# Optimization experiments

Measured on AMD Instinct MI355X. Metric: run time of the kernel, lower is better.

Reference implementation:

```python
import jax, jax.numpy as jnp
import numpy as np

N, OBS, ENC, ACT, K = 16384, 512, 512, 64, 8
ALPHA = 1.0


def setup_inputs() -> dict:
    key = jax.random.key(0)
    ks = jax.random.split(key, 8)
    s = 0.05  # keep activations/logits well-scaled
    return {
        "X1": jax.random.normal(ks[0], (N, OBS), jnp.float32),
        "X0": jax.random.normal(ks[1], (N, OBS), jnp.float32),
        "U": jax.random.normal(ks[2], (N, ACT), jnp.float32),
        "W_enc": jax.random.normal(ks[3], (ENC, OBS), jnp.float32) * s,
        "A_all": jax.random.normal(ks[4], (K, ENC, ENC), jnp.float32) * s,
        "B_rest": jax.random.normal(ks[5], (K - 1, ACT, ENC), jnp.float32) * s,
        "C_w": jax.random.normal(ks[6], (K, ENC), jnp.float32) * s,
        "C_b": jax.random.normal(ks[7], (K,), jnp.float32) * s,
    }


def reference(X1, X0, U, W_enc, A_all, B_rest, C_w, C_b):
    enc_dim = W_enc.shape[0]
    act_dim = U.shape[1]
    k = A_all.shape[0]
    # encoder: bias-free linear
    X1e = X1 @ W_enc.T  # [N, enc]
    X0e = X0 @ W_enc.T  # [N, enc]
    # gating: argmax of linear classifier C
    inds = jnp.argmax(X0e @ C_w.T + C_b, axis=1)  # [N]
    # expert 0 uses fixed B0 = eye(enc)[:act, :]; experts 1..k-1 learned
    B0 = jnp.eye(enc_dim, dtype=X0.dtype)[:act_dim]  # [act, enc]
    B_all = jnp.concatenate([B0[None], B_rest], axis=0)  # [k, act, enc]
    # per-expert predictions for every row (nn.Linear: x @ W.T -> einsum over input dim h)
    preds = jnp.einsum('nh,keh->kne', X0e, A_all) + jnp.einsum('na,kae->kne', U, B_all)
    # squared error per (expert, row), then select each row's routed expert
    sq = jnp.sum((X1e[None, :, :] - preds) ** 2, axis=-1)  # [k, N]
    onehot = jax.nn.one_hot(inds, k, dtype=sq.dtype)  # [N, k]
    loss = ALPHA * jnp.sum(sq * onehot.T)
    return loss / (enc_dim * X1.shape[0])
```

## Files before the change

### kernel.cpp

```cpp
#include <hip/hip_runtime.h>

#define NROWS 16384
#define OBSD 512
#define ENCD 512
#define ACTD 64
#define KEXP 8

typedef __attribute__((ext_vector_type(8))) short bf16x8;
typedef __attribute__((ext_vector_type(4))) float f32x4;
typedef __attribute__((address_space(3))) unsigned char lds_byte;
typedef __attribute__((address_space(1))) unsigned char glb_byte;

__device__ __forceinline__ unsigned short f2bf(float f) {
  unsigned int u = __float_as_uint(f);
  u = (u + 0x7FFFu + ((u >> 16) & 1u)) >> 16;
  return (unsigned short)u;
}
__device__ __forceinline__ float bf2f(unsigned short h) {
  return __uint_as_float(((unsigned int)h) << 16);
}
__device__ __forceinline__ unsigned int cvtpk(float lo, float hi) {
  unsigned int r;
  asm("v_cvt_pk_bf16_f32 %0, %1, %2" : "=v"(r) : "v"(lo), "v"(hi));
  return r;
}
__device__ __forceinline__ void gload_lds16(const unsigned short* g, unsigned short* l) {
  __builtin_amdgcn_global_load_lds((const glb_byte*)g, (lds_byte*)l, 16, 0, 0);
}

__global__ __launch_bounds__(256) void gt_k(
    const float* __restrict__ W, const float* __restrict__ Cw,
    float* __restrict__ GT, float* __restrict__ loss,
    int* __restrict__ counts, int* __restrict__ cursor) {
  const int b = blockIdx.x, tid = threadIdx.x;
  if (b == 0) {
    if (tid == 0) *loss = 0.f;
    if (tid < KEXP) { counts[tid] = 0; cursor[tid] = 0; }
  }
  __shared__ float red[4][64];
  int e = b >> 3, o0 = (b & 7) * 64;
  int o = tid & 63, hg = tid >> 6;
  float s = 0.f;
#pragma unroll 8
  for (int h = hg * 128; h < hg * 128 + 128; h++)
    s += Cw[e * ENCD + h] * W[(size_t)h * OBSD + o0 + o];
  red[hg][o] = s;
  __syncthreads();
  if (tid < 64)
    GT[(o0 + tid) * KEXP + e] = red[0][tid] + red[1][tid] + red[2][tid] + red[3][tid];
}

__global__ __launch_bounds__(256) void fused_prep_k(
    const float* __restrict__ X0, const float* __restrict__ X1,
    const float* __restrict__ U, const float* __restrict__ W,
    const float* __restrict__ Aall, const float* __restrict__ Brest,
    const float* __restrict__ GT, const float* __restrict__ Cb,
    unsigned short* __restrict__ X0bf, unsigned short* __restrict__ X1bf,
    unsigned short* __restrict__ Ubf, unsigned short* __restrict__ Wbf,
    unsigned short* __restrict__ Abf, unsigned short* __restrict__ BfT,
    int* __restrict__ inds, int* __restrict__ counts) {
  const int b = blockIdx.x, tid = threadIdx.x;
  if (b < 512) {
    __shared__ int lhist[KEXP];
    if (tid < KEXP) lhist[tid] = 0;
    __syncthreads();
    const int lane = tid & 63, w = tid >> 6;
    float g[8][8];
    const float* gp = GT + lane * 8 * KEXP;
#pragma unroll
    for (int j = 0; j < 8; j++) {
      float4 lo = *(const float4*)(gp + j * KEXP);
      float4 hi = *(const float4*)(gp + j * KEXP + 4);
      g[j][0] = lo.x; g[j][1] = lo.y; g[j][2] = lo.z; g[j][3] = lo.w;
      g[j][4] = hi.x; g[j][5] = hi.y; g[j][6] = hi.z; g[j][7] = hi.w;
    }
    float cb[KEXP];
#pragma unroll
    for (int e = 0; e < KEXP; e++) cb[e] = Cb[e];
#pragma unroll 2
    for (int r = 0; r < 8; r++) {
      const int n = b * 32 + w * 8 + r;
      const float4* xr = (const float4*)(X0 + (size_t)n * OBSD + lane * 8);
      float4 x = xr[0], y = xr[1];
      float xv[8] = {x.x, x.y, x.z, x.w, y.x, y.y, y.z, y.w};
      float acc[KEXP] = {};
#pragma unroll
      for (int j = 0; j < 8; j++)
#pragma unroll
        for (int e = 0; e < KEXP; e++) acc[e] += xv[j] * g[j][e];
      uint4 rr = {cvtpk(x.x, x.y), cvtpk(x.z, x.w), cvtpk(y.x, y.y), cvtpk(y.z, y.w)};
      *(uint4*)&X0bf[(size_t)n * OBSD + lane * 8] = rr;
#pragma unroll
      for (int e = 0; e < KEXP; e++) {
#pragma unroll
        for (int off = 32; off > 0; off >>= 1) acc[e] += __shfl_xor(acc[e], off, 64);
      }
      if (lane == 0) {
        int best = 0;
        float bv = acc[0] + cb[0];
#pragma unroll
        for (int e = 1; e < KEXP; e++) {
          float v = acc[e] + cb[e];
          if (v > bv) { bv = v; best = e; }
        }
        inds[n] = best;
        atomicAdd(&lhist[best], 1);
      }
    }
    __syncthreads();
    if (tid < KEXP) atomicAdd(&counts[tid], lhist[tid]);
    return;
  }
  if (b < 4608) {
    size_t i = ((size_t)(b - 512) * 256 + tid) * 8;
    const float4* s4 = (const float4*)(X1 + i);
    float4 a = s4[0], c = s4[1];
    uint4 r = {cvtpk(a.x, a.y), cvtpk(a.z, a.w), cvtpk(c.x, c.y), cvtpk(c.z, c.w)};
    *(uint4*)&X1bf[i] = r;
    return;
  }
  if (b < 4664) {
    __shared__ float tile[64][65];
    int t = b - 4608;
    int k = (t >> 3);
    int e0 = (t & 7) * 64;
    const float* src = Brest + (size_t)k * ACTD * ENCD + e0;
#pragma unroll
    for (int j = 0; j < 16; j++) {
      int idx = j * 256 + tid;
      int a = idx >> 6, e = idx & 63;
      tile[a][e] = src[(size_t)a * ENCD + e];
    }
    __syncthreads();
    unsigned short* dst = BfT + ((size_t)(k + 1) * ENCD + e0) * ACTD;
#pragma unroll
    for (int j = 0; j < 16; j++) {
      int idx = j * 256 + tid;
      int e = idx >> 6, a = idx & 63;
      dst[(size_t)e * ACTD + a] = f2bf(tile[a][e]);
    }
    return;
  }
  if (b == 4664) {
    for (int j = 0; j < 16; j++) {
      int i8 = j * 256 + tid;
      int e = i8 >> 3, a0 = (i8 & 7) * 8;
      unsigned int w0 = 0, w1 = 0, w2 = 0, w3 = 0;
      if (e >= a0 && e < a0 + 8) {
        unsigned int bits = 0x3F80u << ((e & 1) * 16);
        if ((e - a0) >> 1 == 0) w0 = bits;
        else if ((e - a0) >> 1 == 1) w1 = bits;
        else if ((e - a0) >> 1 == 2) w2 = bits;
        else w3 = bits;
      }
      uint4 v = {w0, w1, w2, w3};
      *(uint4*)&BfT[(size_t)i8 * 8] = v;
    }
    return;
  }
  int cb2 = b - 4665;
  const float* src;
  unsigned short* dst;
  size_t i;
  if (cb2 < 1024)      { src = U;    dst = Ubf; i = (size_t)cb2 * 256 + tid; }
  else if (cb2 < 1280) { src = W;    dst = Wbf; i = (size_t)(cb2 - 1024) * 256 + tid; }
  else                 { src = Aall; dst = Abf; i = (size_t)(cb2 - 1280) * 256 + tid; }
  float4 v = ((const float4*)src)[i];
  uint2 r = {cvtpk(v.x, v.y), cvtpk(v.z, v.w)};
  *(uint2*)&dst[i * 4] = r;
}

__global__ void prefix_k(const int* __restrict__ counts, int* __restrict__ cursor,
                         int* __restrict__ starts) {
  if (threadIdx.x == 0 && blockIdx.x == 0) {
    int s = 0;
    for (int k = 0; k < KEXP; k++) { starts[k] = s; cursor[k] = s; s += counts[k]; }
    starts[KEXP] = s;
  }
}

__global__ __launch_bounds__(256, 2) void enc_scatter_k(
    const unsigned short* __restrict__ X1bf, const unsigned short* __restrict__ X0bf,
    const unsigned short* __restrict__ Wbf, unsigned short* __restrict__ X1e,
    unsigned short* __restrict__ X0e, const int* __restrict__ inds,
    int* __restrict__ cursor, int* __restrict__ rowlist) {
  if (blockIdx.x >= 1024) {
    __shared__ int lhist[KEXP], lbase[KEXP];
    const int tid = threadIdx.x;
    if (tid < KEXP) lhist[tid] = 0;
    __syncthreads();
    const int n = (blockIdx.x - 1024) * 256 + tid;
    const int r = inds[n];
    const int lpos = atomicAdd(&lhist[r], 1);
    __syncthreads();
    if (tid < KEXP) lbase[tid] = atomicAdd(&cursor[tid], lhist[tid]);
    __syncthreads();
    rowlist[lbase[r] + lpos] = n;
    return;
  }
  __shared__ unsigned short As[128 * 64];
  __shared__ unsigned short Bs[128 * 64];
  const int tid = threadIdx.x;
  const int bid = blockIdx.x;
  const int lid = (bid & 7) * 128 + (bid >> 3);
  const int lz = lid >> 9;
  const int rem = lid & 511;
  const int col0 = (rem & 3) * 128;
  const int row0 = (rem >> 2) * 128;
  const unsigned short* X = lz ? X0bf : X1bf;
  unsigned short* E = lz ? X0e : X1e;

  const int lane = tid & 63, w = tid >> 6;
  const int wr = w >> 1, wc = w & 1;
  const int srow8 = tid >> 3;
  const int lslot = ((tid & 7) ^ (srow8 & 7)) * 8;
  const int ldsoff = tid * 8;
  const int r15 = lane & 15;
  const int qk = lane >> 4;
  const int rsw = r15 & 7;
  const int arow = wr * 64 + r15;
  const int brow = wc * 64 + r15;

  f32x4 acc[4][4] = {};
  for (int k0 = 0; k0 < OBSD; k0 += 64) {
#pragma unroll
    for (int j = 0; j < 4; j++) {
      int row = j * 32 + srow8;
      gload_lds16(X + (size_t)(row0 + row) * OBSD + k0 + lslot, &As[j * 2048 + ldsoff]);
      gload_lds16(Wbf + (size_t)(col0 + row) * OBSD + k0 + lslot, &Bs[j * 2048 + ldsoff]);
    }
    __syncthreads();
#pragma unroll
    for (int kk = 0; kk < 2; kk++) {
      const int ps = ((kk * 4 + qk) ^ rsw) * 8;
      bf16x8 af[4], bfr[4];
#pragma unroll
      for (int m = 0; m < 4; m++) af[m] = *(const bf16x8*)&As[(arow + m * 16) * 64 + ps];
#pragma unroll
      for (int n = 0; n < 4; n++) bfr[n] = *(const bf16x8*)&Bs[(brow + n * 16) * 64 + ps];
#pragma unroll
      for (int m = 0; m < 4; m++)
#pragma unroll
        for (int n = 0; n < 4; n++)
          acc[m][n] = __builtin_amdgcn_mfma_f32_16x16x32_bf16(bfr[n], af[m], acc[m][n], 0, 0, 0);
    }
    __syncthreads();
  }
#pragma unroll
  for (int m = 0; m < 4; m++) {
    int rowg = row0 + wr * 64 + m * 16 + r15;
#pragma unroll
    for (int n = 0; n < 4; n++) {
      int colg = col0 + wc * 64 + n * 16 + qk * 4;
      uint2 v = {cvtpk(acc[m][n][0], acc[m][n][1]), cvtpk(acc[m][n][2], acc[m][n][3])};
      *(uint2*)&E[(size_t)rowg * ENCD + colg] = v;
    }
  }
}

__global__ __launch_bounds__(256, 2) void grouped_mfma_k(
    const unsigned short* __restrict__ X0ebf, const unsigned short* __restrict__ X1ebf,
    const unsigned short* __restrict__ Ubf, const unsigned short* __restrict__ Abf,
    const unsigned short* __restrict__ BfTbf, const int* __restrict__ rowlist,
    const int* __restrict__ starts, float* __restrict__ loss) {
  const int tid = threadIdx.x;
  const int bid = blockIdx.x;
  const int lid = (bid & 7) * 512 + (bid >> 3);
  const int k = lid >> 9;
  const int rem = lid & 511;
  const int col0 = (rem & 3) * 128;
  const int tile = rem >> 2;

  const int start = starts[k];
  const int cnt = starts[k + 1] - start;
  if (tile * 128 >= cnt) return;

  __shared__ unsigned short As[128 * 32];
  __shared__ unsigned short Bs[128 * 32];
  __shared__ int ridx[128];
  __shared__ float red[4];

  if (tid < 128) {
    int p = tile * 128 + tid;
    ridx[tid] = rowlist[start + (p < cnt ? p : 0)];
  }
  __syncthreads();

  const int lane = tid & 63, w = tid >> 6;
  const int wr = w >> 1, wc = w & 1;
  const int gslot = ((tid & 3) ^ ((tid >> 3) & 3)) * 8;
  const int srow = tid >> 2;
  const int ldsoff = tid * 8;
  const int rslot = ((lane >> 4) ^ (((lane & 15) >> 1) & 3)) * 8;
  const int arow = wr * 64 + (lane & 15);
  const int brow = wc * 64 + (lane & 15);
  const int rn0 = ridx[srow];
  const int rn1 = ridx[64 + srow];

  f32x4 acc[4][4] = {};
  const unsigned short* Ak = Abf + (size_t)k * ENCD * ENCD;
  for (int k0 = 0; k0 < ENCD; k0 += 32) {
    gload_lds16(X0ebf + (size_t)rn0 * ENCD + k0 + gslot, &As[ldsoff]);
    gload_lds16(X0ebf + (size_t)rn1 * ENCD + k0 + gslot, &As[2048 + ldsoff]);
    gload_lds16(Ak + (size_t)(col0 + srow) * ENCD + k0 + gslot, &Bs[ldsoff]);
    gload_lds16(Ak + (size_t)(col0 + 64 + srow) * ENCD + k0 + gslot, &Bs[2048 + ldsoff]);
    __syncthreads();
    bf16x8 af[4], bfr[4];
#pragma unroll
    for (int m = 0; m < 4; m++) af[m] = *(const bf16x8*)&As[(arow + m * 16) * 32 + rslot];
#pragma unroll
    for (int n = 0; n < 4; n++) bfr[n] = *(const bf16x8*)&Bs[(brow + n * 16) * 32 + rslot];
#pragma unroll
    for (int m = 0; m < 4; m++)
#pragma unroll
      for (int n = 0; n < 4; n++)
        acc[m][n] = __builtin_amdgcn_mfma_f32_16x16x32_bf16(bfr[n], af[m], acc[m][n], 0, 0, 0);
    __syncthreads();
  }
  const unsigned short* BfTk = BfTbf + (size_t)k * ENCD * ACTD;
  for (int a0 = 0; a0 < ACTD; a0 += 32) {
    gload_lds16(Ubf + (size_t)rn0 * ACTD + a0 + gslot, &As[ldsoff]);
    gload_lds16(Ubf + (size_t)rn1 * ACTD + a0 + gslot, &As[2048 + ldsoff]);
    gload_lds16(BfTk + (size_t)(col0 + srow) * ACTD + a0 + gslot, &Bs[ldsoff]);
    gload_lds16(BfTk + (size_t)(col0 + 64 + srow) * ACTD + a0 + gslot, &Bs[2048 + ldsoff]);
    __syncthreads();
    bf16x8 af[4], bfr[4];
#pragma unroll
    for (int m = 0; m < 4; m++) af[m] = *(const bf16x8*)&As[(arow + m * 16) * 32 + rslot];
#pragma unroll
    for (int n = 0; n < 4; n++) bfr[n] = *(const bf16x8*)&Bs[(brow + n * 16) * 32 + rslot];
#pragma unroll
    for (int m = 0; m < 4; m++)
#pragma unroll
      for (int n = 0; n < 4; n++)
        acc[m][n] = __builtin_amdgcn_mfma_f32_16x16x32_bf16(bfr[n], af[m], acc[m][n], 0, 0, 0);
    __syncthreads();
  }
  float sq = 0.f;
#pragma unroll
  for (int m = 0; m < 4; m++) {
    int lr = wr * 64 + m * 16 + (lane & 15);
    bool valid = (tile * 128 + lr) < cnt;
    const unsigned short* xrow = X1ebf + (size_t)ridx[lr] * ENCD;
#pragma unroll
    for (int n = 0; n < 4; n++) {
      int cg = col0 + wc * 64 + n * 16 + (lane >> 4) * 4;
      if (valid) {
        ushort4 x4 = *(const ushort4*)&xrow[cg];
        float d0 = bf2f(x4.x) - acc[m][n][0];
        float d1 = bf2f(x4.y) - acc[m][n][1];
        float d2 = bf2f(x4.z) - acc[m][n][2];
        float d3 = bf2f(x4.w) - acc[m][n][3];
        sq += d0 * d0 + d1 * d1 + d2 * d2 + d3 * d3;
      }
    }
  }
#pragma unroll
  for (int off = 32; off > 0; off >>= 1) sq += __shfl_xor(sq, off, 64);
  if (lane == 0) red[w] = sq;
  __syncthreads();
  if (tid == 0) atomicAdd(loss, red[0] + red[1] + red[2] + red[3]);
}

__global__ void finalize_k(const float* __restrict__ loss, float* __restrict__ out) {
  if (threadIdx.x == 0 && blockIdx.x == 0)
    out[0] = loss[0] * (1.0f / ((float)ENCD * (float)NROWS));
}

extern "C" void kernel_launch(void* const* d_in, const int* in_sizes, int n_in,
                              void* d_out, int out_size, void* d_ws, size_t ws_size,
                              hipStream_t stream) {
  const float* X1 = (const float*)d_in[0];
  const float* X0 = (const float*)d_in[1];
  const float* U = (const float*)d_in[2];
  const float* W = (const float*)d_in[3];
  const float* Aall = (const float*)d_in[4];
  const float* Brest = (const float*)d_in[5];
  const float* Cw = (const float*)d_in[6];
  const float* Cb = (const float*)d_in[7];
  float* out = (float*)d_out;

  char* p = (char*)d_ws;
  auto alloc = [&](size_t bytes) { char* r = p; p += (bytes + 255) & ~(size_t)255; return r; };
  unsigned short* X1bf = (unsigned short*)alloc((size_t)NROWS * OBSD * 2);
  unsigned short* X0bf = (unsigned short*)alloc((size_t)NROWS * OBSD * 2);
  unsigned short* Ubf = (unsigned short*)alloc((size_t)NROWS * ACTD * 2);
  unsigned short* Wbf = (unsigned short*)alloc((size_t)ENCD * OBSD * 2);
  unsigned short* Abf = (unsigned short*)alloc((size_t)KEXP * ENCD * ENCD * 2);
  unsigned short* BfT = (unsigned short*)alloc((size_t)KEXP * ENCD * ACTD * 2);
  unsigned short* X1ebf = (unsigned short*)alloc((size_t)NROWS * ENCD * 2);
  unsigned short* X0ebf = (unsigned short*)alloc((size_t)NROWS * ENCD * 2);
  float* GT = (float*)alloc(KEXP * OBSD * 4);
  float* loss = (float*)alloc(256);
  int* inds = (int*)alloc(NROWS * 4);
  int* rowlist = (int*)alloc(NROWS * 4);
  int* counts = (int*)alloc(64);
  int* cursor = (int*)alloc(64);
  int* starts = (int*)alloc(64);

  gt_k<<<64, 256, 0, stream>>>(W, Cw, GT, loss, counts, cursor);
  fused_prep_k<<<7993, 256, 0, stream>>>(X0, X1, U, W, Aall, Brest, GT, Cb,
                                         X0bf, X1bf, Ubf, Wbf, Abf, BfT,
                                         inds, counts);
  prefix_k<<<1, 1, 0, stream>>>(counts, cursor, starts);
  enc_scatter_k<<<1088, 256, 0, stream>>>(X1bf, X0bf, Wbf, X1ebf, X0ebf,
                                          inds, cursor, rowlist);
  grouped_mfma_k<<<4096, 256, 0, stream>>>(X0ebf, X1ebf, Ubf, Abf, BfT,
                                           rowlist, starts, loss);
  finalize_k<<<1, 64, 0, stream>>>(loss, out);
}
```

Measured before the change: 87.80 us.

## Fuse X1 encoding into grouped expert GEMM via negated expert weights

X1 is no longer encoded in a separate GEMM pass that writes X1e. The grouped kernel now accumulates X1@W^T, then adds X0e@(-A_k)^T and U@(-B_k)^T into the same accumulator, so the residual comes straight out of the MFMA and the loss is just its squared sum. This removes half the encoder GEMM and the X1e write and read-back, at the cost of a longer K loop per tile (OBS+ENC+ACT) and re-reading W per tile. The K-step also grows from 32 to 64 with wider swizzled LDS tiles.

Measured after the change: 83.73 us. -4.6%, faster.

```diff
diff --git a/kernel.cpp b/kernel.cpp
--- a/kernel.cpp
+++ b/kernel.cpp
@@ -15,9 +15,6 @@
   unsigned int u = __float_as_uint(f);
   u = (u + 0x7FFFu + ((u >> 16) & 1u)) >> 16;
   return (unsigned short)u;
-}
-__device__ __forceinline__ float bf2f(unsigned short h) {
-  return __uint_as_float(((unsigned int)h) << 16);
 }
 __device__ __forceinline__ unsigned int cvtpk(float lo, float hi) {
   unsigned int r;
@@ -57,7 +54,7 @@
     const float* __restrict__ GT, const float* __restrict__ Cb,
     unsigned short* __restrict__ X0bf, unsigned short* __restrict__ X1bf,
     unsigned short* __restrict__ Ubf, unsigned short* __restrict__ Wbf,
-    unsigned short* __restrict__ Abf, unsigned short* __restrict__ BfT,
+    unsigned short* __restrict__ AbfN, unsigned short* __restrict__ BfTN,
     int* __restrict__ inds, int* __restrict__ counts) {
   const int b = blockIdx.x, tid = threadIdx.x;
   if (b < 512) {
@@ -132,12 +129,12 @@
       tile[a][e] = src[(size_t)a * ENCD + e];
     }
     __syncthreads();
-    unsigned short* dst = BfT + ((size_t)(k + 1) * ENCD + e0) * ACTD;
+    unsigned short* dst = BfTN + ((size_t)(k + 1) * ENCD + e0) * ACTD;
 #pragma unroll
     for (int j = 0; j < 16; j++) {
       int idx = j * 256 + tid;
       int e = idx >> 6, a = idx & 63;
-      dst[(size_t)e * ACTD + a] = f2bf(tile[a][e]);
+      dst[(size_t)e * ACTD + a] = f2bf(-tile[a][e]);
     }
     return;
   }
@@ -147,27 +144,34 @@
       int e = i8 >> 3, a0 = (i8 & 7) * 8;
       unsigned int w0 = 0, w1 = 0, w2 = 0, w3 = 0;
       if (e >= a0 && e < a0 + 8) {
-        unsigned int bits = 0x3F80u << ((e & 1) * 16);
+        unsigned int bits = 0xBF80u << ((e & 1) * 16);
         if ((e - a0) >> 1 == 0) w0 = bits;
         else if ((e - a0) >> 1 == 1) w1 = bits;
         else if ((e - a0) >> 1 == 2) w2 = bits;
         else w3 = bits;
       }
       uint4 v = {w0, w1, w2, w3};
-      *(uint4*)&BfT[(size_t)i8 * 8] = v;
+      *(uint4*)&BfTN[(size_t)i8 * 8] = v;
     }
     return;
   }
   int cb2 = b - 4665;
-  const float* src;
-  unsigned short* dst;
-  size_t i;
-  if (cb2 < 1024)      { src = U;    dst = Ubf; i = (size_t)cb2 * 256 + tid; }
-  else if (cb2 < 1280) { src = W;    dst = Wbf; i = (size_t)(cb2 - 1024) * 256 + tid; }
-  else                 { src = Aall; dst = Abf; i = (size_t)(cb2 - 1280) * 256 + tid; }
-  float4 v = ((const float4*)src)[i];
-  uint2 r = {cvtpk(v.x, v.y), cvtpk(v.z, v.w)};
-  *(uint2*)&dst[i * 4] = r;
+  if (cb2 < 1024) {
+    size_t i = (size_t)cb2 * 256 + tid;
+    float4 v = ((const float4*)U)[i];
+    uint2 r = {cvtpk(v.x, v.y), cvtpk(v.z, v.w)};
+    *(uint2*)&Ubf[i * 4] = r;
+  } else if (cb2 < 1280) {
+    size_t i = (size_t)(cb2 - 1024) * 256 + tid;
+    float4 v = ((const float4*)W)[i];
+    uint2 r = {cvtpk(v.x, v.y), cvtpk(v.z, v.w)};
+    *(uint2*)&Wbf[i * 4] = r;
+  } else {
+    size_t i = (size_t)(cb2 - 1280) * 256 + tid;
+    float4 v = ((const float4*)Aall)[i];
+    uint2 r = {cvtpk(-v.x, -v.y), cvtpk(-v.z, -v.w)};
+    *(uint2*)&AbfN[i * 4] = r;
+  }
 }
 
 __global__ void prefix_k(const int* __restrict__ counts, int* __restrict__ cursor,
@@ -180,16 +184,15 @@
 }
 
 __global__ __launch_bounds__(256, 2) void enc_scatter_k(
-    const unsigned short* __restrict__ X1bf, const unsigned short* __restrict__ X0bf,
-    const unsigned short* __restrict__ Wbf, unsigned short* __restrict__ X1e,
+    const unsigned short* __restrict__ X0bf, const unsigned short* __restrict__ Wbf,
     unsigned short* __restrict__ X0e, const int* __restrict__ inds,
     int* __restrict__ cursor, int* __restrict__ rowlist) {
-  if (blockIdx.x >= 1024) {
+  if (blockIdx.x >= 512) {
     __shared__ int lhist[KEXP], lbase[KEXP];
     const int tid = threadIdx.x;
     if (tid < KEXP) lhist[tid] = 0;
     __syncthreads();
-    const int n = (blockIdx.x - 1024) * 256 + tid;
+    const int n = (blockIdx.x - 512) * 256 + tid;
     const int r = inds[n];
     const int lpos = atomicAdd(&lhist[r], 1);
     __syncthreads();
@@ -202,13 +205,9 @@
   __shared__ unsigned short Bs[128 * 64];
   const int tid = threadIdx.x;
   const int bid = blockIdx.x;
-  const int lid = (bid & 7) * 128 + (bid >> 3);
-  const int lz = lid >> 9;
-  const int rem = lid & 511;
-  const int col0 = (rem & 3) * 128;
-  const int row0 = (rem >> 2) * 128;
-  const unsigned short* X = lz ? X0bf : X1bf;
-  unsigned short* E = lz ? X0e : X1e;
+  const int lid = (bid & 7) * 64 + (bid >> 3);
+  const int col0 = (lid & 3) * 128;
+  const int row0 = (lid >> 2) * 128;
 
   const int lane = tid & 63, w = tid >> 6;
   const int wr = w >> 1, wc = w & 1;
@@ -226,7 +225,7 @@
 #pragma unroll
     for (int j = 0; j < 4; j++) {
       int row = j * 32 + srow8;
-      gload_lds16(X + (size_t)(row0 + row) * OBSD + k0 + lslot, &As[j * 2048 + ldsoff]);
+      gload_lds16(X0bf + (size_t)(row0 + row) * OBSD + k0 + lslot, &As[j * 2048 + ldsoff]);
       gload_lds16(Wbf + (size_t)(col0 + row) * OBSD + k0 + lslot, &Bs[j * 2048 + ldsoff]);
     }
     __syncthreads();
@@ -253,16 +252,17 @@
     for (int n = 0; n < 4; n++) {
       int colg = col0 + wc * 64 + n * 16 + qk * 4;
       uint2 v = {cvtpk(acc[m][n][0], acc[m][n][1]), cvtpk(acc[m][n][2], acc[m][n][3])};
-      *(uint2*)&E[(size_t)rowg * ENCD + colg] = v;
+      *(uint2*)&X0e[(size_t)rowg * ENCD + colg] = v;
     }
   }
 }
 
 __global__ __launch_bounds__(256, 2) void grouped_mfma_k(
-    const unsigned short* __restrict__ X0ebf, const unsigned short* __restrict__ X1ebf,
-    const unsigned short* __restrict__ Ubf, const unsigned short* __restrict__ Abf,
-    const unsigned short* __restrict__ BfTbf, const int* __restrict__ rowlist,
-    const int* __restrict__ starts, float* __restrict__ loss) {
+    const unsigned short* __restrict__ X1bf, const unsigned short* __restrict__ X0ebf,
+    const unsigned short* __restrict__ Wbf, const unsigned short* __restrict__ Ubf,
+    const unsigned short* __restrict__ AbfN, const unsigned short* __restrict__ BfTN,
+    const int* __restrict__ rowlist, const int* __restrict__ starts,
+    float* __restrict__ loss) {
   const int tid = threadIdx.x;
   const int bid = blockIdx.x;
   const int lid = (bid & 7) * 512 + (bid >> 3);
@@ -275,8 +275,8 @@
   const int cnt = starts[k + 1] - start;
   if (tile * 128 >= cnt) return;
 
-  __shared__ unsigned short As[128 * 32];
-  __shared__ unsigned short Bs[128 * 32];
+  __shared__ unsigned short As[128 * 64];
+  __shared__ unsigned short Bs[128 * 64];
   __shared__ int ridx[128];
   __shared__ float red[4];
 
@@ -288,71 +288,78 @@
 
   const int lane = tid & 63, w = tid >> 6;
   const int wr = w >> 1, wc = w & 1;
-  const int gslot = ((tid & 3) ^ ((tid >> 3) & 3)) * 8;
-  const int srow = tid >> 2;
+  const int srow8 = tid >> 3;
+  const int lslot = ((tid & 7) ^ (srow8 & 7)) * 8;
   const int ldsoff = tid * 8;
-  const int rslot = ((lane >> 4) ^ (((lane & 15) >> 1) & 3)) * 8;
-  const int arow = wr * 64 + (lane & 15);
-  const int brow = wc * 64 + (lane & 15);
-  const int rn0 = ridx[srow];
-  const int rn1 = ridx[64 + srow];
+  const int r15 = lane & 15;
+  const int qk = lane >> 4;
+  const int rsw = r15 & 7;
+  const int arow = wr * 64 + r15;
+  const int brow = wc * 64 + r15;
+  int rnj[4];
+#pragma unroll
+  for (int j = 0; j < 4; j++) rnj[j] = ridx[j * 32 + srow8];
+
+  const unsigned short* AkN = AbfN + (size_t)k * ENCD * ENCD;
+  const unsigned short* BfTkN = BfTN + (size_t)k * ENCD * ACTD;
 
   f32x4 acc[4][4] = {};
-  const unsigned short* Ak = Abf + (size_t)k * ENCD * ENCD;
-  for (int k0 = 0; k0 < ENCD; k0 += 32) {
-    gload_lds16(X0ebf + (size_t)rn0 * ENCD + k0 + gslot, &As[ldsoff]);
-    gload_lds16(X0ebf + (size_t)rn1 * ENCD + k0 + gslot, &As[2048 + ldsoff]);
-    gload_lds16(Ak + (size_t)(col0 + srow) * ENCD + k0 + gslot, &Bs[ldsoff]);
-    gload_lds16(Ak + (size_t)(col0 + 64 + srow) * ENCD + k0 + gslot, &Bs[2048 + ldsoff]);
-    __syncthreads();
-    bf16x8 af[4], bfr[4];
-#pragma unroll
-    for (int m = 0; m < 4; m++) af[m] = *(const bf16x8*)&As[(arow + m * 16) * 32 + rslot];
-#pragma unroll
-    for (int n = 0; n < 4; n++) bfr[n] = *(const bf16x8*)&Bs[(brow + n * 16) * 32 + rslot];
-#pragma unroll
-    for (int m = 0; m < 4; m++)
+#define GROUPED_COMPUTE()                                                            \
+  do {                                                                               \
+    __syncthreads();                                                                 \
+    _Pragma("unroll") for (int kk = 0; kk < 2; kk++) {                               \
+      const int ps = ((kk * 4 + qk) ^ rsw) * 8;                                      \
+      bf16x8 af[4], bfr[4];                                                          \
+      _Pragma("unroll") for (int m = 0; m < 4; m++)                                  \
+          af[m] = *(const bf16x8*)&As[(arow + m * 16) * 64 + ps];                    \
+      _Pragma("unroll") for (int n = 0; n < 4; n++)                                  \
+          bfr[n] = *(const bf16x8*)&Bs[(brow + n * 16) * 64 + ps];                   \
+      _Pragma("unroll") for (int m = 0; m < 4; m++)                                  \
+          _Pragma("unroll") for (int n = 0; n < 4; n++)                              \
+              acc[m][n] = __builtin_amdgcn_mfma_f32_16x16x32_bf16(bfr[n], af[m],     \
+                                                                  acc[m][n], 0, 0, 0); \
+    }                                                                                \
+    __syncthreads();                                                                 \
+  } while (0)
+
+  for (int k0 = 0; k0 < ENCD; k0 += 64) {
+#pragma unroll
+    for (int j = 0; j < 4; j++) {
+      int row = j * 32 + srow8;
+      gload_lds16(X1bf + (size_t)rnj[j] * OBSD + k0 + lslot, &As[j * 2048 + ldsoff]);
+      gload_lds16(Wbf + (size_t)(col0 + row) * OBSD + k0 + lslot, &Bs[j * 2048 + ldsoff]);
+    }
+    GROUPED_COMPUTE();
+  }
+  for (int k0 = 0; k0 < ENCD; k0 += 64) {
+#pragma unroll
+    for (int j = 0; j < 4; j++) {
+      int row = j * 32 + srow8;
+      gload_lds16(X0ebf + (size_t)rnj[j] * ENCD + k0 + lslot, &As[j * 2048 + ldsoff]);
+      gload_lds16(AkN + (size_t)(col0 + row) * ENCD + k0 + lslot, &Bs[j * 2048 + ldsoff]);
+    }
+    GROUPED_COMPUTE();
+  }
+  {
+#pragma unroll
+    for (int j = 0; j < 4; j++) {
+      int row = j * 32 + srow8;
+      gload_lds16(Ubf + (size_t)rnj[j] * ACTD + lslot, &As[j * 2048 + ldsoff]);
+      gload_lds16(BfTkN + (size_t)(col0 + row) * ACTD + lslot, &Bs[j * 2048 + ldsoff]);
+    }
+    GROUPED_COMPUTE();
+  }
+#undef GROUPED_COMPUTE
+
+  float sq = 0.f;
+#pragma unroll
+  for (int m = 0; m < 4; m++) {
+    int lr = wr * 64 + m * 16 + r15;
+    if (tile * 128 + lr < cnt) {
 #pragma unroll
       for (int n = 0; n < 4; n++)
-        acc[m][n] = __builtin_amdgcn_mfma_f32_16x16x32_bf16(bfr[n], af[m], acc[m][n], 0, 0, 0);
-    __syncthreads();
-  }
-  const unsigned short* BfTk = BfTbf + (size_t)k * ENCD * ACTD;
-  for (int a0 = 0; a0 < ACTD; a0 += 32) {
-    gload_lds16(Ubf + (size_t)rn0 * ACTD + a0 + gslot, &As[ldsoff]);
-    gload_lds16(Ubf + (size_t)rn1 * ACTD + a0 + gslot, &As[2048 + ldsoff]);
-    gload_lds16(BfTk + (size_t)(col0 + srow) * ACTD + a0 + gslot, &Bs[ldsoff]);
-    gload_lds16(BfTk + (size_t)(col0 + 64 + srow) * ACTD + a0 + gslot, &Bs[2048 + ldsoff]);
-    __syncthreads();
-    bf16x8 af[4], bfr[4];
-#pragma unroll
-    for (int m = 0; m < 4; m++) af[m] = *(const bf16x8*)&As[(arow + m * 16) * 32 + rslot];
-#pragma unroll
-    for (int n = 0; n < 4; n++) bfr[n] = *(const bf16x8*)&Bs[(brow + n * 16) * 32 + rslot];
-#pragma unroll
-    for (int m = 0; m < 4; m++)
-#pragma unroll
-      for (int n = 0; n < 4; n++)
-        acc[m][n] = __builtin_amdgcn_mfma_f32_16x16x32_bf16(bfr[n], af[m], acc[m][n], 0, 0, 0);
-    __syncthreads();
-  }
-  float sq = 0.f;
-#pragma unroll
-  for (int m = 0; m < 4; m++) {
-    int lr = wr * 64 + m * 16 + (lane & 15);
-    bool valid = (tile * 128 + lr) < cnt;
-    const unsigned short* xrow = X1ebf + (size_t)ridx[lr] * ENCD;
-#pragma unroll
-    for (int n = 0; n < 4; n++) {
-      int cg = col0 + wc * 64 + n * 16 + (lane >> 4) * 4;
-      if (valid) {
-        ushort4 x4 = *(const ushort4*)&xrow[cg];
-        float d0 = bf2f(x4.x) - acc[m][n][0];
-        float d1 = bf2f(x4.y) - acc[m][n][1];
-        float d2 = bf2f(x4.z) - acc[m][n][2];
-        float d3 = bf2f(x4.w) - acc[m][n][3];
-        sq += d0 * d0 + d1 * d1 + d2 * d2 + d3 * d3;
-      }
+        sq += acc[m][n][0] * acc[m][n][0] + acc[m][n][1] * acc[m][n][1] +
+              acc[m][n][2] * acc[m][n][2] + acc[m][n][3] * acc[m][n][3];
     }
   }
 #pragma unroll
@@ -386,9 +393,8 @@
   unsigned short* X0bf = (unsigned short*)alloc((size_t)NROWS * OBSD * 2);
   unsigned short* Ubf = (unsigned short*)alloc((size_t)NROWS * ACTD * 2);
   unsigned short* Wbf = (unsigned short*)alloc((size_t)ENCD * OBSD * 2);
-  unsigned short* Abf = (unsigned short*)alloc((size_t)KEXP * ENCD * ENCD * 2);
-  unsigned short* BfT = (unsigned short*)alloc((size_t)KEXP * ENCD * ACTD * 2);
-  unsigned short* X1ebf = (unsigned short*)alloc((size_t)NROWS * ENCD * 2);
+  unsigned short* AbfN = (unsigned short*)alloc((size_t)KEXP * ENCD * ENCD * 2);
+  unsigned short* BfTN = (unsigned short*)alloc((size_t)KEXP * ENCD * ACTD * 2);
   unsigned short* X0ebf = (unsigned short*)alloc((size_t)NROWS * ENCD * 2);
   float* GT = (float*)alloc(KEXP * OBSD * 4);
   float* loss = (float*)alloc(256);
@@ -400,12 +406,11 @@
 
   gt_k<<<64, 256, 0, stream>>>(W, Cw, GT, loss, counts, cursor);
   fused_prep_k<<<7993, 256, 0, stream>>>(X0, X1, U, W, Aall, Brest, GT, Cb,
-                                         X0bf, X1bf, Ubf, Wbf, Abf, BfT,
+                                         X0bf, X1bf, Ubf, Wbf, AbfN, BfTN,
                                          inds, counts);
   prefix_k<<<1, 1, 0, stream>>>(counts, cursor, starts);
-  enc_scatter_k<<<1088, 256, 0, stream>>>(X1bf, X0bf, Wbf, X1ebf, X0ebf,
-                                          inds, cursor, rowlist);
-  grouped_mfma_k<<<4096, 256, 0, stream>>>(X0ebf, X1ebf, Ubf, Abf, BfT,
+  enc_scatter_k<<<576, 256, 0, stream>>>(X0bf, Wbf, X0ebf, inds, cursor, rowlist);
+  grouped_mfma_k<<<4096, 256, 0, stream>>>(X1bf, X0ebf, Wbf, Ubf, AbfN, BfTN,
                                            rowlist, starts, loss);
   finalize_k<<<1, 64, 0, stream>>>(loss, out);
 }
```
